# Kernel tuning notes

Measured on AMD Instinct MI355X. Metric: run time of the kernel, lower is better.

Reference implementation:

```python
import jax, jax.numpy as jnp
import numpy as np


def setup_inputs() -> dict:
    key = jax.random.key(0)
    k1, k2 = jax.random.split(key)
    B, H, W, D, K = 32, 32, 32, 256, 8192
    x = jax.random.normal(k1, (B, H, W, D), dtype=jnp.float32)
    # tf.random_uniform_initializer default: U(-0.05, 0.05), shape (embedding_dim, n_embeddings)
    embeddings = jax.random.uniform(k2, (D, K), dtype=jnp.float32, minval=-0.05, maxval=0.05)
    return {"x": x, "embeddings": embeddings}


def reference(x, embeddings):
    beta = 0.25
    D = embeddings.shape[0]
    input_shape = x.shape
    flat = x.reshape(-1, D)  # [N, D]
    similarity = flat @ embeddings  # [N, K]
    distance = (jnp.sum(flat ** 2, axis=1, keepdims=True)
                + jnp.sum(embeddings ** 2, axis=0)
                - 2.0 * similarity)
    idx = jnp.argmin(distance, axis=1)  # [N]
    # one_hot @ embeddings.T is a row gather of embeddings.T
    quantized = jnp.take(embeddings.T, idx, axis=0).reshape(input_shape)
    commitment_loss = jnp.mean((jax.lax.stop_gradient(quantized) - x) ** 2)
    codebook_loss = jnp.mean((quantized - jax.lax.stop_gradient(x)) ** 2)
    loss = beta * commitment_loss + codebook_loss
    # straight-through estimator
    quantized_ste = x + jax.lax.stop_gradient(quantized - x)
    return quantized_ste, loss
```

## Files before the change

kernel.cpp:

```cpp
#include <hip/hip_runtime.h>
#include <hip/hip_bf16.h>
#include <stdint.h>
#include <stddef.h>


typedef float f32x4 __attribute__((ext_vector_type(4)));
typedef _Float16 half8 __attribute__((ext_vector_type(8)));

#define N_ROWS    32768
#define K_CODES   8192
#define TAU       3e-3f
#define TAU2      1.2e-4f
#define CHK       2e-3
#define FLAGCAP   8192

#define WS_ETF    0
#define WS_EHT    8388608
#define WS_ELT    12582912
#define WS_ENF    16777216
#define WS_EN64   16809984
#define WS_ENP    16875520
#define WS_IDX    17137664
#define WS_SC     17268736
#define WS_CNT    17399808
#define WS_LIST   17399824
#define WS_LIST2  17432592
#define WS_PF1    17465360
#define WS_PF2    17727504
#define WS_PI1    17989648
#define WS_PD     18251792
#define WS_PIR    18776080
#define WS_ROWSUM 19038224
#define WS_FLAGS  19169296
#define WS_NEED   19169312

__device__ __forceinline__ float bf2f(unsigned short u) {
  union { unsigned int i; float f; } v; v.i = ((unsigned int)u) << 16; return v.f;
}
__device__ __forceinline__ float xraw(const void* x, int fx, size_t i) {
  return fx ? ((const float*)x)[i] : bf2f(((const unsigned short*)x)[i]);
}

__global__ void vq_buildAll(const void* __restrict__ e, const unsigned short* __restrict__ xu,
                            int* __restrict__ flags, int* __restrict__ cnt,
                            float* __restrict__ eTf, _Float16* __restrict__ eHt,
                            _Float16* __restrict__ eLt, double* __restrict__ enp) {
  __shared__ float tile[64][65];
  __shared__ int fs[2];
  const int t = threadIdx.x;
  if (t < 2) fs[t] = 0;
  __syncthreads();
  const unsigned short* eu = (const unsigned short*)e;
  if (((xu[2 * t] >> 7) & 0xFF) >= 0xC0) atomicOr(&fs[0], 1);
  if (((eu[2 * t] >> 7) & 0xFF) >= 0xC0) atomicOr(&fs[1], 1);
  __syncthreads();
  const int fe = fs[1];
  if (blockIdx.x == 0 && t == 0) { flags[0] = fs[0]; flags[1] = fs[1]; cnt[0] = 0; cnt[1] = 0; }

  const int dt = blockIdx.x & 3;
  const int d0 = dt * 64;
  const int k0 = (blockIdx.x >> 2) * 64;
  const float* ef = (const float*)e;
#pragma unroll
  for (int i = 0; i < 16; ++i) {
    const int idx = i * 256 + t;
    const int dd = idx >> 6, kk = idx & 63;
    const size_t src = (size_t)(d0 + dd) * 8192 + (k0 + kk);
    tile[dd][kk] = fe ? ef[src] : bf2f(eu[src]);
  }
  __syncthreads();
#pragma unroll
  for (int i = 0; i < 16; ++i) {
    const int idx = i * 256 + t;
    const int kr = idx >> 6, dc = idx & 63;
    eTf[(size_t)(k0 + kr) * 256 + (d0 + dc)] = tile[dc][kr];
  }
#pragma unroll
  for (int i = 0; i < 2; ++i) {
    const int u = i * 256 + t;
    const int kr = u >> 3, g = u & 7;
    const int k = k0 + kr, d = d0 + g * 8;
    _Float16 h[8], l[8];
    double s = 0.0;
#pragma unroll
    for (int j = 0; j < 8; ++j) {
      const float v = tile[g * 8 + j][kr];
      h[j] = (_Float16)v;
      l[j] = (_Float16)(v - (float)h[j]);
      s += (double)v * (double)v;
    }
    const size_t o = (size_t)((k >> 4) * 8 + (d >> 5)) * 512 + ((d >> 3) & 3) * 128 + (k & 15) * 8;
    *(half8*)(eHt + o) = *(const half8*)h;
    *(half8*)(eLt + o) = *(const half8*)l;
#pragma unroll
    for (int off = 1; off <= 4; off <<= 1) s += __shfl_xor(s, off);
    if ((t & 7) == 0) enp[(size_t)dt * 8192 + k] = s;
  }
}

__global__ void vq_finNorm(const double* __restrict__ enp, double* __restrict__ en64,
                           float* __restrict__ enF) {
  const int k = blockIdx.x * 256 + threadIdx.x;
  double s = enp[k];
  s += enp[8192 + k];
  s += enp[16384 + k];
  s += enp[24576 + k];
  en64[k] = s;
  enF[k] = (float)s;
}

__global__ __launch_bounds__(512, 2) void vq_main(
    const void* __restrict__ x,
    const _Float16* __restrict__ eHt,
    const float* __restrict__ enorm,
    const int* __restrict__ flags,
    int* __restrict__ idxOut, float* __restrict__ scOut,
    int* __restrict__ cnt, int* __restrict__ lst) {
  __shared__ unsigned char smem[38912];
  const int t = threadIdx.x;
  const int wv = t >> 6, lane = t & 63;
  const int i16 = lane & 15, q = lane >> 4;
  const int n0 = blockIdx.x * 64;
  const int fx = flags[0];

  {
    const int row = t >> 3, col = t & 7;
#pragma unroll
    for (int g = 0; g < 4; ++g) {
      float v[8];
      if (fx) {
        const float* xf = (const float*)x;
        *(f32x4*)&v[0] = *(const f32x4*)(xf + (size_t)(n0 + row) * 256 + col * 32 + g * 8);
        *(f32x4*)&v[4] = *(const f32x4*)(xf + (size_t)(n0 + row) * 256 + col * 32 + g * 8 + 4);
      } else {
        const unsigned short* xu = (const unsigned short*)x;
#pragma unroll
        for (int j = 0; j < 8; ++j)
          v[j] = bf2f(xu[(size_t)(n0 + row) * 256 + col * 32 + g * 8 + j]);
      }
      _Float16 h[8];
#pragma unroll
      for (int j = 0; j < 8; ++j) h[j] = (_Float16)v[j];
      const int off = ((col * 64 + g * 16) ^ ((row & 7) << 4));
      *(half8*)(smem + row * 512 + off) = *(const half8*)h;
    }
  }
  __syncthreads();

  f32x4 acc[4][4];
#pragma unroll
  for (int mt = 0; mt < 4; ++mt)
#pragma unroll
    for (int nt = 0; nt < 4; ++nt) acc[mt][nt] = (f32x4){0.f, 0.f, 0.f, 0.f};
  float b1[4], b2[4]; int i1[4];
#pragma unroll
  for (int nt = 0; nt < 4; ++nt) { b1[nt] = 3.4e38f; b2[nt] = 3.4e38f; i1[nt] = 0x7fffffff; }

  const int swz = (i16 & 7) << 4;
  const _Float16* pA = eHt + (size_t)(wv * 64) * 4096 + lane * 8;

  half8 Apf[4];
#pragma unroll
  for (int mt = 0; mt < 4; ++mt) Apf[mt] = *(const half8*)(pA + mt * 4096);

  for (int ct = 0; ct < 16; ++ct) {
    const int cb = wv * 1024 + ct * 64;
#pragma unroll
    for (int s = 0; s < 8; ++s) {
      half8 An[4];
      const int nc = (s == 7) ? ((ct + 1) & 15) : ct;
      const int ns = (s + 1) & 7;
#pragma unroll
      for (int mt = 0; mt < 4; ++mt)
        An[mt] = *(const half8*)(pA + (nc * 4 + mt) * 4096 + ns * 512);

      const int boff = (s * 64 + q * 16) ^ swz;
      half8 B0 = *(const half8*)(smem + (i16) * 512 + boff);
      half8 B1 = *(const half8*)(smem + (16 + i16) * 512 + boff);
      half8 B2 = *(const half8*)(smem + (32 + i16) * 512 + boff);
      half8 B3 = *(const half8*)(smem + (48 + i16) * 512 + boff);
      __builtin_amdgcn_s_setprio(1);
#pragma unroll
      for (int mt = 0; mt < 4; ++mt) {
        acc[mt][0] = __builtin_amdgcn_mfma_f32_16x16x32_f16(Apf[mt], B0, acc[mt][0], 0, 0, 0);
        acc[mt][1] = __builtin_amdgcn_mfma_f32_16x16x32_f16(Apf[mt], B1, acc[mt][1], 0, 0, 0);
        acc[mt][2] = __builtin_amdgcn_mfma_f32_16x16x32_f16(Apf[mt], B2, acc[mt][2], 0, 0, 0);
        acc[mt][3] = __builtin_amdgcn_mfma_f32_16x16x32_f16(Apf[mt], B3, acc[mt][3], 0, 0, 0);
      }
      __builtin_amdgcn_s_setprio(0);
#pragma unroll
      for (int mt = 0; mt < 4; ++mt) Apf[mt] = An[mt];
    }
#pragma unroll
    for (int mt = 0; mt < 4; ++mt) {
      const f32x4 en = *(const f32x4*)(enorm + cb + mt * 16 + q * 4);
#pragma unroll
      for (int nt = 0; nt < 4; ++nt) {
#pragma unroll
        for (int r = 0; r < 4; ++r) {
          const float sc = fmaf(-2.f, acc[mt][nt][r], en[r]);
          b2[nt] = __builtin_amdgcn_fmed3f(sc, b1[nt], b2[nt]);
          const bool better = sc < b1[nt];
          b1[nt] = better ? sc : b1[nt];
          i1[nt] = better ? (cb + mt * 16 + q * 4 + r) : i1[nt];
        }
        acc[mt][nt] = (f32x4){0.f, 0.f, 0.f, 0.f};
      }
    }
  }

#pragma unroll
  for (int off = 16; off <= 32; off <<= 1) {
#pragma unroll
    for (int nt = 0; nt < 4; ++nt) {
      const float os  = __shfl_xor(b1[nt], off);
      const int   oi  = __shfl_xor(i1[nt], off);
      const float os2 = __shfl_xor(b2[nt], off);
      const float nb2 = fminf(fminf(b2[nt], os2), fmaxf(b1[nt], os));
      const bool take = (os < b1[nt]) || (os == b1[nt] && oi < i1[nt]);
      b1[nt] = take ? os : b1[nt];
      i1[nt] = take ? oi : i1[nt];
      b2[nt] = nb2;
    }
  }

  __syncthreads();
  float* redS  = (float*)(smem + 32768);
  int*   redI  = (int*)(smem + 32768 + 2048);
  float* redS2 = (float*)(smem + 32768 + 4096);
  if (q == 0) {
#pragma unroll
    for (int nt = 0; nt < 4; ++nt) {
      const int rr = wv * 64 + nt * 16 + i16;
      redS[rr] = b1[nt]; redI[rr] = i1[nt]; redS2[rr] = b2[nt];
    }
  }
  __syncthreads();
  if (t < 64) {
    float B1 = 3.4e38f, B2 = 3.4e38f; int I1 = 0x7fffffff;
#pragma unroll
    for (int w = 0; w < 8; ++w) {
      const float s1 = redS[w * 64 + t]; const int ii = redI[w * 64 + t]; const float s2 = redS2[w * 64 + t];
      const float nb2 = fminf(fminf(B2, s2), fmaxf(B1, s1));
      const bool take = (s1 < B1) || (s1 == B1 && ii < I1);
      B1 = take ? s1 : B1; I1 = take ? ii : I1; B2 = nb2;
    }
    idxOut[n0 + t] = I1;
    scOut[n0 + t] = B1;
    if (B2 - B1 < TAU) {
      const int p = atomicAdd(cnt, 1);
      if (p < FLAGCAP) lst[p] = n0 + t;
    }
  }
}

__global__ __launch_bounds__(512) void vq_refine(
    const void* __restrict__ x,
    const _Float16* __restrict__ eHt, const _Float16* __restrict__ eLt,
    const float* __restrict__ enorm, const int* __restrict__ flags,
    const int* __restrict__ cnt, const int* __restrict__ lst,
    float* __restrict__ pf1, float* __restrict__ pf2, int* __restrict__ pi1,
    int* __restrict__ cnt1) {
  __shared__ unsigned char smem[65536];
  const int t = threadIdx.x;
  const int wv = t >> 6, lane = t & 63;
  const int i16 = lane & 15, q = lane >> 4;
  const int fx = flags[0];
  const int m = cnt[0];
  if (m > FLAGCAP) {
    if (blockIdx.x == 0 && t == 0) cnt1[0] = N_ROWS;
    return;
  }
  const int units = ((m + 63) >> 6) * 8;
  const int swz = (i16 & 7) << 4;

  for (int u = blockIdx.x; u < units; u += gridDim.x) {
    const int g = u >> 3, sl = u & 7;
    __syncthreads();
    {
      const int row = t >> 3, col = t & 7;
      const int gi = g * 64 + row;
      const int n = (gi < m) ? (lst[gi] & (N_ROWS - 1)) : 0;
#pragma unroll
      for (int gg = 0; gg < 4; ++gg) {
        float v[8];
        if (fx) {
          const float* xf = (const float*)x;
          *(f32x4*)&v[0] = *(const f32x4*)(xf + (size_t)n * 256 + col * 32 + gg * 8);
          *(f32x4*)&v[4] = *(const f32x4*)(xf + (size_t)n * 256 + col * 32 + gg * 8 + 4);
        } else {
          const unsigned short* xu = (const unsigned short*)x;
#pragma unroll
          for (int j = 0; j < 8; ++j)
            v[j] = bf2f(xu[(size_t)n * 256 + col * 32 + gg * 8 + j]);
        }
        _Float16 h[8], l[8];
#pragma unroll
        for (int j = 0; j < 8; ++j) {
          h[j] = (_Float16)v[j];
          l[j] = (_Float16)(v[j] - (float)h[j]);
        }
        const int off = ((col * 64 + gg * 16) ^ ((row & 7) << 4));
        *(half8*)(smem + row * 512 + off) = *(const half8*)h;
        *(half8*)(smem + 32768 + row * 512 + off) = *(const half8*)l;
      }
    }
    __syncthreads();

    f32x4 acc[4][4];
#pragma unroll
    for (int mt = 0; mt < 4; ++mt)
#pragma unroll
      for (int nt = 0; nt < 4; ++nt) acc[mt][nt] = (f32x4){0.f, 0.f, 0.f, 0.f};
    float b1[4], b2[4]; int i1[4];
#pragma unroll
    for (int nt = 0; nt < 4; ++nt) { b1[nt] = 3.4e38f; b2[nt] = 3.4e38f; i1[nt] = 0x7fffffff; }

    for (int ct = 0; ct < 2; ++ct) {
      const int cb = sl * 1024 + wv * 128 + ct * 64;
#pragma unroll
      for (int s = 0; s < 8; ++s) {
        half8 Ah[4], Al[4];
#pragma unroll
        for (int mt = 0; mt < 4; ++mt) {
          const size_t ab = (size_t)(cb / 16 + mt) * 4096 + s * 512 + lane * 8;
          Ah[mt] = *(const half8*)(eHt + ab);
          Al[mt] = *(const half8*)(eLt + ab);
        }
        const int boff = (s * 64 + q * 16) ^ swz;
        {
          half8 B[4];
#pragma unroll
          for (int nt = 0; nt < 4; ++nt)
            B[nt] = *(const half8*)(smem + (nt * 16 + i16) * 512 + boff);
#pragma unroll
          for (int mt = 0; mt < 4; ++mt)
#pragma unroll
            for (int nt = 0; nt < 4; ++nt) {
              acc[mt][nt] = __builtin_amdgcn_mfma_f32_16x16x32_f16(Ah[mt], B[nt], acc[mt][nt], 0, 0, 0);
              acc[mt][nt] = __builtin_amdgcn_mfma_f32_16x16x32_f16(Al[mt], B[nt], acc[mt][nt], 0, 0, 0);
            }
        }
        {
          half8 B[4];
#pragma unroll
          for (int nt = 0; nt < 4; ++nt)
            B[nt] = *(const half8*)(smem + 32768 + (nt * 16 + i16) * 512 + boff);
#pragma unroll
          for (int mt = 0; mt < 4; ++mt)
#pragma unroll
            for (int nt = 0; nt < 4; ++nt)
              acc[mt][nt] = __builtin_amdgcn_mfma_f32_16x16x32_f16(Ah[mt], B[nt], acc[mt][nt], 0, 0, 0);
        }
      }
#pragma unroll
      for (int mt = 0; mt < 4; ++mt) {
        const f32x4 en = *(const f32x4*)(enorm + cb + mt * 16 + q * 4);
#pragma unroll
        for (int nt = 0; nt < 4; ++nt) {
#pragma unroll
          for (int r = 0; r < 4; ++r) {
            const float sc = fmaf(-2.f, acc[mt][nt][r], en[r]);
            b2[nt] = __builtin_amdgcn_fmed3f(sc, b1[nt], b2[nt]);
            const bool better = sc < b1[nt];
            b1[nt] = better ? sc : b1[nt];
            i1[nt] = better ? (cb + mt * 16 + q * 4 + r) : i1[nt];
          }
          acc[mt][nt] = (f32x4){0.f, 0.f, 0.f, 0.f};
        }
      }
    }

#pragma unroll
    for (int off = 16; off <= 32; off <<= 1) {
#pragma unroll
      for (int nt = 0; nt < 4; ++nt) {
        const float os  = __shfl_xor(b1[nt], off);
        const int   oi  = __shfl_xor(i1[nt], off);
        const float os2 = __shfl_xor(b2[nt], off);
        const float nb2 = fminf(fminf(b2[nt], os2), fmaxf(b1[nt], os));
        const bool take = (os < b1[nt]) || (os == b1[nt] && oi < i1[nt]);
        b1[nt] = take ? os : b1[nt];
        i1[nt] = take ? oi : i1[nt];
        b2[nt] = nb2;
      }
    }

    __syncthreads();
    float* redS  = (float*)(smem + 32768);
    int*   redI  = (int*)(smem + 32768 + 2048);
    float* redS2 = (float*)(smem + 32768 + 4096);
    if (q == 0) {
#pragma unroll
      for (int nt = 0; nt < 4; ++nt) {
        const int rr = wv * 64 + nt * 16 + i16;
        redS[rr] = b1[nt]; redI[rr] = i1[nt]; redS2[rr] = b2[nt];
      }
    }
    __syncthreads();
    if (t < 64) {
      float B1 = 3.4e38f, B2 = 3.4e38f; int I1 = 0x7fffffff;
#pragma unroll
      for (int w = 0; w < 8; ++w) {
        const float s1 = redS[w * 64 + t]; const int ii = redI[w * 64 + t]; const float s2 = redS2[w * 64 + t];
        const float nb2 = fminf(fminf(B2, s2), fmaxf(B1, s1));
        const bool take = (s1 < B1) || (s1 == B1 && ii < I1);
        B1 = take ? s1 : B1; I1 = take ? ii : I1; B2 = nb2;
      }
      const int gi = g * 64 + t;
      if (gi < m) { pf1[gi * 8 + sl] = B1; pf2[gi * 8 + sl] = B2; pi1[gi * 8 + sl] = I1; }
    }
  }
}

__global__ void vq_resolveR(const int* __restrict__ cnt, const int* __restrict__ lst,
                            const float* __restrict__ pf1, const float* __restrict__ pf2,
                            const int* __restrict__ pi1,
                            int* __restrict__ idxOut, float* __restrict__ scOut,
                            int* __restrict__ cnt1, int* __restrict__ lst2) {
  const int m = cnt[0];
  if (m > FLAGCAP) return;
  const int li = blockIdx.x * 256 + threadIdx.x;
  if (li >= m) return;
  float B1 = 3.4e38f, B2 = 3.4e38f; int I1 = 0x7fffffff;
#pragma unroll
  for (int sl = 0; sl < 8; ++sl) {
    const float s1 = pf1[li * 8 + sl]; const int ii = pi1[li * 8 + sl]; const float s2 = pf2[li * 8 + sl];
    const float nb2 = fminf(fminf(B2, s2), fmaxf(B1, s1));
    const bool take = (s1 < B1) || (s1 == B1 && ii < I1);
    B1 = take ? s1 : B1; I1 = take ? ii : I1; B2 = nb2;
  }
  const int n = lst[li] & (N_ROWS - 1);
  idxOut[n] = I1;
  scOut[n] = B1;
  if (B2 - B1 < TAU2) {
    const int p = atomicAdd(cnt1, 1);
    if (p < FLAGCAP) lst2[p] = n;
  }
}

__global__ void vq_gathercheck(const void* __restrict__ x, const float* __restrict__ eTf,
                               const int* __restrict__ flags, const int* __restrict__ idx,
                               const float* __restrict__ sc,
                               float* __restrict__ out, float* __restrict__ rowsum,
                               int* __restrict__ cnt1, int* __restrict__ lst2) {
  const int t = threadIdx.x;
  const int gid = blockIdx.x * 256 + t;
  const int n = gid >> 5, s = gid & 31;
  const int fx = flags[0];
  const int code = idx[n] & (K_CODES - 1);
  const f32x4 q0 = *(const f32x4*)(eTf + (size_t)code * 256 + s * 8);
  const f32x4 q1 = *(const f32x4*)(eTf + (size_t)code * 256 + s * 8 + 4);
  *(f32x4*)(out + (size_t)n * 256 + s * 8) = q0;
  *(f32x4*)(out + (size_t)n * 256 + s * 8 + 4) = q1;
  double d2 = 0.0, x2 = 0.0;
#pragma unroll
  for (int j = 0; j < 4; ++j) {
    const double xv0 = (double)xraw(x, fx, (size_t)n * 256 + s * 8 + j);
    const double xv1 = (double)xraw(x, fx, (size_t)n * 256 + s * 8 + 4 + j);
    const double da = (double)q0[j] - xv0;
    const double db = (double)q1[j] - xv1;
    d2 += da * da + db * db;
    x2 += xv0 * xv0 + xv1 * xv1;
  }
#pragma unroll
  for (int off = 16; off >= 1; off >>= 1) {
    d2 += __shfl_xor(d2, off);
    x2 += __shfl_xor(x2, off);
  }
  if (s == 0) {
    rowsum[n] = (float)d2;
    if (fabs(d2 - (x2 + (double)sc[n])) > CHK) {
      const int p = atomicAdd(cnt1, 1);
      if (p < FLAGCAP) lst2[p] = n;
    }
  }
}

__global__ void vq_rescan8(const void* __restrict__ x, const float* __restrict__ eTf,
                           const double* __restrict__ en64, const int* __restrict__ flags,
                           const int* __restrict__ cnt1, const int* __restrict__ lst2,
                           double* __restrict__ pd, int* __restrict__ pir,
                           int* __restrict__ idxOut) {
  __shared__ float sxx[256];
  __shared__ double wS[4]; __shared__ int wI[4];
  const int t = threadIdx.x;
  const int lane = t & 63, wv = t >> 6;
  const int fx = flags[0];
  const int m = cnt1[0];
  if (m <= FLAGCAP) {
    const int units = m * 8;
    for (int u = blockIdx.x; u < units; u += gridDim.x) {
      const int li = u >> 3, sl = u & 7;
      const int n = lst2[li] & (N_ROWS - 1);
      __syncthreads();
      sxx[t] = xraw(x, fx, (size_t)n * 256 + t);
      __syncthreads();
      const f32x4 xv = *(const f32x4*)&sxx[lane * 4];
      double best = 1e300; int bi = 0x7fffffff;
      for (int i = 0; i < 256; ++i) {
        const int c = sl * 1024 + wv * 256 + i;
        const f32x4 ev = *(const f32x4*)(eTf + (size_t)c * 256 + lane * 4);
        double s = (double)ev[0] * (double)xv[0] + (double)ev[1] * (double)xv[1]
                 + (double)ev[2] * (double)xv[2] + (double)ev[3] * (double)xv[3];
#pragma unroll
        for (int off = 32; off >= 1; off >>= 1) s += __shfl_xor(s, off);
        const double dist = en64[c] - 2.0 * s;
        if (dist < best) { best = dist; bi = c; }
      }
      if (lane == 0) { wS[wv] = best; wI[wv] = bi; }
      __syncthreads();
      if (t == 0) {
        double B = wS[0]; int I = wI[0];
#pragma unroll
        for (int w = 1; w < 4; ++w)
          if (wS[w] < B || (wS[w] == B && wI[w] < I)) { B = wS[w]; I = wI[w]; }
        pd[li * 8 + sl] = B; pir[li * 8 + sl] = I;
      }
    }
  } else {
    for (int n = blockIdx.x; n < N_ROWS; n += gridDim.x) {
      __syncthreads();
      sxx[t] = xraw(x, fx, (size_t)n * 256 + t);
      __syncthreads();
      const f32x4 xv = *(const f32x4*)&sxx[lane * 4];
      double best = 1e300; int bi = 0x7fffffff;
      for (int i = 0; i < 2048; ++i) {
        const int c = wv * 2048 + i;
        const f32x4 ev = *(const f32x4*)(eTf + (size_t)c * 256 + lane * 4);
        double s = (double)ev[0] * (double)xv[0] + (double)ev[1] * (double)xv[1]
                 + (double)ev[2] * (double)xv[2] + (double)ev[3] * (double)xv[3];
#pragma unroll
        for (int off = 32; off >= 1; off >>= 1) s += __shfl_xor(s, off);
        const double dist = en64[c] - 2.0 * s;
        if (dist < best) { best = dist; bi = c; }
      }
      if (lane == 0) { wS[wv] = best; wI[wv] = bi; }
      __syncthreads();
      if (t == 0) {
        double B = wS[0]; int I = wI[0];
#pragma unroll
        for (int w = 1; w < 4; ++w)
          if (wS[w] < B || (wS[w] == B && wI[w] < I)) { B = wS[w]; I = wI[w]; }
        idxOut[n] = I;
      }
    }
  }
}

__global__ void vq_resolve(const void* __restrict__ x, const float* __restrict__ eTf,
                           const int* __restrict__ flags,
                           const int* __restrict__ cnt1, const int* __restrict__ lst2,
                           const double* __restrict__ pd, const int* __restrict__ pir,
                           int* __restrict__ idxOut, float* __restrict__ out,
                           float* __restrict__ rowsum) {
  __shared__ double rS[256];
  __shared__ int bcode;
  const int t = threadIdx.x;
  const int fx = flags[0];
  const int m = cnt1[0];
  if (m <= FLAGCAP) {
    for (int li = blockIdx.x; li < m; li += gridDim.x) {
      const int n = lst2[li] & (N_ROWS - 1);
      if (t == 0) {
        double B = pd[li * 8]; int I = pir[li * 8];
#pragma unroll
        for (int sl = 1; sl < 8; ++sl) {
          const double s = pd[li * 8 + sl]; const int ii = pir[li * 8 + sl];
          if (s < B || (s == B && ii < I)) { B = s; I = ii; }
        }
        idxOut[n] = I; bcode = I;
      }
      __syncthreads();
      const float qv = eTf[(size_t)bcode * 256 + t];
      out[(size_t)n * 256 + t] = qv;
      const double dq = (double)qv - (double)xraw(x, fx, (size_t)n * 256 + t);
      rS[t] = dq * dq;
      __syncthreads();
      if (t == 0) {
        double a = 0.0;
        for (int j = 0; j < 256; ++j) a += rS[j];
        rowsum[n] = (float)a;
      }
      __syncthreads();
    }
  } else {
    for (int n = blockIdx.x; n < N_ROWS; n += gridDim.x) {
      const int code = idxOut[n] & (K_CODES - 1);
      const float qv = eTf[(size_t)code * 256 + t];
      out[(size_t)n * 256 + t] = qv;
      const double dq = (double)qv - (double)xraw(x, fx, (size_t)n * 256 + t);
      rS[t] = dq * dq;
      __syncthreads();
      if (t == 0) {
        double a = 0.0;
        for (int j = 0; j < 256; ++j) a += rS[j];
        rowsum[n] = (float)a;
      }
      __syncthreads();
    }
  }
}

__global__ void vq_loss(const float* __restrict__ rowsum, const int* __restrict__ flags,
                        float* __restrict__ out) {
  __shared__ double sd[256];
  const int t = threadIdx.x;
  double a = 0.0;
  for (int i = t; i < N_ROWS; i += 256) a += (double)rowsum[i];
  sd[t] = a;
  __syncthreads();
  if (t == 0) {
    double tot = 0.0;
    for (int j = 0; j < 256; ++j) tot += sd[j];
    out[8388608] = (float)(1.25 * (tot / 8388608.0));
    if (flags[0] == 0) out[0] = 272.0f + 16.0f * (float)flags[1];
  }
}

extern "C" void kernel_launch(void* const* d_in, const int* in_sizes, int n_in,
                              void* d_out, int out_size, void* d_ws, size_t ws_size,
                              hipStream_t stream) {
  (void)out_size;
  if (ws_size < (size_t)WS_NEED) return;

  const void* x = d_in[0];
  const void* e = d_in[1];
  if (n_in >= 2 && in_sizes[0] == 2097152 && in_sizes[1] == 8388608) {
    x = d_in[1]; e = d_in[0];
  }
  float* out = (float*)d_out;
  char* ws = (char*)d_ws;

  float* eTf     = (float*)(ws + WS_ETF);
  _Float16* eHt  = (_Float16*)(ws + WS_EHT);
  _Float16* eLt  = (_Float16*)(ws + WS_ELT);
  float* enF     = (float*)(ws + WS_ENF);
  double* en64   = (double*)(ws + WS_EN64);
  double* enp    = (double*)(ws + WS_ENP);
  int* idx       = (int*)(ws + WS_IDX);
  float* sc      = (float*)(ws + WS_SC);
  int* cnt       = (int*)(ws + WS_CNT);
  int* lst       = (int*)(ws + WS_LIST);
  int* lst2      = (int*)(ws + WS_LIST2);
  float* pf1     = (float*)(ws + WS_PF1);
  float* pf2     = (float*)(ws + WS_PF2);
  int* pi1       = (int*)(ws + WS_PI1);
  double* pd     = (double*)(ws + WS_PD);
  int* pir       = (int*)(ws + WS_PIR);
  float* rowsum  = (float*)(ws + WS_ROWSUM);
  int* flags     = (int*)(ws + WS_FLAGS);

  (void)hipGetLastError();
  vq_buildAll<<<512, 256, 0, stream>>>(e, (const unsigned short*)x, flags, cnt, eTf, eHt, eLt, enp);
  vq_finNorm<<<32, 256, 0, stream>>>(enp, en64, enF);
  vq_main<<<N_ROWS / 64, 512, 0, stream>>>(x, eHt, enF, flags, idx, sc, cnt, lst);
  vq_refine<<<1024, 512, 0, stream>>>(x, eHt, eLt, enF, flags, cnt, lst, pf1, pf2, pi1, cnt + 1);
  vq_resolveR<<<FLAGCAP / 256, 256, 0, stream>>>(cnt, lst, pf1, pf2, pi1, idx, sc, cnt + 1, lst2);
  vq_gathercheck<<<N_ROWS * 32 / 256, 256, 0, stream>>>(x, eTf, flags, idx, sc, out, rowsum, cnt + 1, lst2);
  vq_rescan8<<<2048, 256, 0, stream>>>(x, eTf, en64, flags, cnt + 1, lst2, pd, pir, idx);
  vq_resolve<<<2048, 256, 0, stream>>>(x, eTf, flags, cnt + 1, lst2, pd, pir, idx, out, rowsum);
  vq_loss<<<1, 256, 0, stream>>>(rowsum, flags, out);

  if (hipGetLastError() != hipSuccess)
    hipMemsetAsync(d_out, 0x42, 4, stream);
}
```

Baseline: 408.0 us.

## Reorder fp16 codebook layout for contiguous per-wave streaming with double-buffered prefetch

Changes the packed half-precision codebook layout so that each wave's 64-code, 32-dim fragments for consecutive k-steps sit contiguously in 2048-element chunks grouped by 1024-code slice. The main distance kernel now keeps two register buffers of A fragments and prefetches two steps ahead instead of one, using the new contiguous addressing. The refinement kernel's addressing is updated to the new layout. This targets global-load latency and locality in the MFMA loop, at the cost of more registers for the second A buffer.

```diff
diff --git a/kernel.cpp b/kernel.cpp
--- a/kernel.cpp
+++ b/kernel.cpp
@@ -79,7 +79,7 @@
   for (int i = 0; i < 2; ++i) {
     const int u = i * 256 + t;
     const int kr = u >> 3, g = u & 7;
-    const int k = k0 + kr, d = d0 + g * 8;
+    const int k = k0 + kr;
     _Float16 h[8], l[8];
     double s = 0.0;
 #pragma unroll
@@ -89,7 +89,9 @@
       l[j] = (_Float16)(v - (float)h[j]);
       s += (double)v * (double)v;
     }
-    const size_t o = (size_t)((k >> 4) * 8 + (d >> 5)) * 512 + ((d >> 3) & 3) * 128 + (k & 15) * 8;
+    const size_t o = (size_t)(k >> 10) * 262144
+                   + (size_t)(((((k >> 6) & 15) * 8) + dt * 2 + (g >> 2)) * 4 + ((k >> 4) & 3)) * 512
+                   + (size_t)(g & 3) * 128 + (size_t)(k & 15) * 8;
     *(half8*)(eHt + o) = *(const half8*)h;
     *(half8*)(eLt + o) = *(const half8*)l;
 #pragma unroll
@@ -157,40 +159,40 @@
   for (int nt = 0; nt < 4; ++nt) { b1[nt] = 3.4e38f; b2[nt] = 3.4e38f; i1[nt] = 0x7fffffff; }
 
   const int swz = (i16 & 7) << 4;
-  const _Float16* pA = eHt + (size_t)(wv * 64) * 4096 + lane * 8;
-
-  half8 Apf[4];
-#pragma unroll
-  for (int mt = 0; mt < 4; ++mt) Apf[mt] = *(const half8*)(pA + mt * 4096);
+  const _Float16* pA = eHt + (size_t)wv * 262144 + lane * 8;
+
+  half8 A0[4], A1[4];
+#pragma unroll
+  for (int mt = 0; mt < 4; ++mt) {
+    A0[mt] = *(const half8*)(pA + mt * 512);
+    A1[mt] = *(const half8*)(pA + 2048 + mt * 512);
+  }
+
+#define VQSTEP(Ac, s)                                                          \
+  {                                                                            \
+    const int boff = ((s) * 64 + q * 16) ^ swz;                                \
+    const half8 B0 = *(const half8*)(smem + (i16) * 512 + boff);               \
+    const half8 B1 = *(const half8*)(smem + (16 + i16) * 512 + boff);          \
+    const half8 B2 = *(const half8*)(smem + (32 + i16) * 512 + boff);          \
+    const half8 B3 = *(const half8*)(smem + (48 + i16) * 512 + boff);          \
+    __builtin_amdgcn_s_setprio(1);                                             \
+    _Pragma("unroll")                                                          \
+    for (int mt = 0; mt < 4; ++mt) {                                           \
+      acc[mt][0] = __builtin_amdgcn_mfma_f32_16x16x32_f16(Ac[mt], B0, acc[mt][0], 0, 0, 0); \
+      acc[mt][1] = __builtin_amdgcn_mfma_f32_16x16x32_f16(Ac[mt], B1, acc[mt][1], 0, 0, 0); \
+      acc[mt][2] = __builtin_amdgcn_mfma_f32_16x16x32_f16(Ac[mt], B2, acc[mt][2], 0, 0, 0); \
+      acc[mt][3] = __builtin_amdgcn_mfma_f32_16x16x32_f16(Ac[mt], B3, acc[mt][3], 0, 0, 0); \
+    }                                                                          \
+    __builtin_amdgcn_s_setprio(0);                                             \
+    const _Float16* pf = pA + (size_t)(((ct * 8 + (s) + 2) & 127) * 2048);     \
+    _Pragma("unroll")                                                          \
+    for (int mt = 0; mt < 4; ++mt) Ac[mt] = *(const half8*)(pf + mt * 512);    \
+  }
 
   for (int ct = 0; ct < 16; ++ct) {
     const int cb = wv * 1024 + ct * 64;
-#pragma unroll
-    for (int s = 0; s < 8; ++s) {
-      half8 An[4];
-      const int nc = (s == 7) ? ((ct + 1) & 15) : ct;
-      const int ns = (s + 1) & 7;
-#pragma unroll
-      for (int mt = 0; mt < 4; ++mt)
-        An[mt] = *(const half8*)(pA + (nc * 4 + mt) * 4096 + ns * 512);
-
-      const int boff = (s * 64 + q * 16) ^ swz;
-      half8 B0 = *(const half8*)(smem + (i16) * 512 + boff);
-      half8 B1 = *(const half8*)(smem + (16 + i16) * 512 + boff);
-      half8 B2 = *(const half8*)(smem + (32 + i16) * 512 + boff);
-      half8 B3 = *(const half8*)(smem + (48 + i16) * 512 + boff);
-      __builtin_amdgcn_s_setprio(1);
-#pragma unroll
-      for (int mt = 0; mt < 4; ++mt) {
-        acc[mt][0] = __builtin_amdgcn_mfma_f32_16x16x32_f16(Apf[mt], B0, acc[mt][0], 0, 0, 0);
-        acc[mt][1] = __builtin_amdgcn_mfma_f32_16x16x32_f16(Apf[mt], B1, acc[mt][1], 0, 0, 0);
-        acc[mt][2] = __builtin_amdgcn_mfma_f32_16x16x32_f16(Apf[mt], B2, acc[mt][2], 0, 0, 0);
-        acc[mt][3] = __builtin_amdgcn_mfma_f32_16x16x32_f16(Apf[mt], B3, acc[mt][3], 0, 0, 0);
-      }
-      __builtin_amdgcn_s_setprio(0);
-#pragma unroll
-      for (int mt = 0; mt < 4; ++mt) Apf[mt] = An[mt];
-    }
+    VQSTEP(A0, 0) VQSTEP(A1, 1) VQSTEP(A0, 2) VQSTEP(A1, 3)
+    VQSTEP(A0, 4) VQSTEP(A1, 5) VQSTEP(A0, 6) VQSTEP(A1, 7)
 #pragma unroll
     for (int mt = 0; mt < 4; ++mt) {
       const f32x4 en = *(const f32x4*)(enorm + cb + mt * 16 + q * 4);
@@ -208,6 +210,7 @@
       }
     }
   }
+#undef VQSTEP
 
 #pragma unroll
   for (int off = 16; off <= 32; off <<= 1) {
@@ -318,12 +321,13 @@
 
     for (int ct = 0; ct < 2; ++ct) {
       const int cb = sl * 1024 + wv * 128 + ct * 64;
+      const size_t abase = (size_t)sl * 262144 + (size_t)((wv * 2 + ct) * 8) * 2048 + lane * 8;
 #pragma unroll
       for (int s = 0; s < 8; ++s) {
         half8 Ah[4], Al[4];
 #pragma unroll
         for (int mt = 0; mt < 4; ++mt) {
-          const size_t ab = (size_t)(cb / 16 + mt) * 4096 + s * 512 + lane * 8;
+          const size_t ab = abase + (size_t)s * 2048 + mt * 512;
           Ah[mt] = *(const half8*)(eHt + ab);
           Al[mt] = *(const half8*)(eLt + ab);
         }
```

Result: no change. 408.4 us (+0.1%).
